# Kernel tuning notes

Measured on AMD Instinct MI355X. Metric: run time of the kernel, lower is better.

## Reference

```python
import jax, jax.numpy as jnp
import numpy as np

N_HEADS = 16
LEVELS = 3
DS = 2          # downsampling_factor
WINDOW = 128    # sliding window size
B, L, E = 32, 512, 1024


def _mha(q, k, v, Wq, bq, Wk, bk, Wv, bv, Wo, bo):
    """batch_first nn.MultiheadAttention equivalent (no mask)."""
    b, lq, e = q.shape
    lk = k.shape[1]
    d = e // N_HEADS
    scale = 1.0 / np.sqrt(d)
    qh = (q @ Wq + bq).reshape(b, lq, N_HEADS, d)
    kh = (k @ Wk + bk).reshape(b, lk, N_HEADS, d)
    vh = (v @ Wv + bv).reshape(b, lk, N_HEADS, d)
    att = jax.nn.softmax(jnp.einsum('bqhd,bkhd->bhqk', qh, kh) * scale, axis=-1)
    out = jnp.einsum('bhqk,bkhd->bqhd', att, vh).reshape(b, lq, e)
    return out @ Wo + bo


def _downsample(x):
    b, l, e = x.shape
    ln = l // DS
    return x[:, :ln * DS].reshape(b, ln, DS, e).mean(axis=2)


def setup_inputs() -> dict:
    key = jax.random.key(0)
    ks = jax.random.split(key, 8)
    s = E ** -0.5
    return {
        'query': jax.random.normal(ks[0], (B, L, E), jnp.float32),
        'key': jax.random.normal(ks[1], (B, L, E), jnp.float32),
        'value': jax.random.normal(ks[2], (B, L, E), jnp.float32),
        'Wq': jax.random.normal(ks[3], (E, E), jnp.float32) * s,
        'bq': jnp.zeros((E,), jnp.float32),
        'Wk': jax.random.normal(ks[4], (E, E), jnp.float32) * s,
        'bk': jnp.zeros((E,), jnp.float32),
        'Wv': jax.random.normal(ks[5], (E, E), jnp.float32) * s,
        'bv': jnp.zeros((E,), jnp.float32),
        'Wo': jax.random.normal(ks[6], (E, E), jnp.float32) * s,
        'bo': jnp.zeros((E,), jnp.float32),
        'soft_mask': jnp.ones((L,), jnp.float32),
    }


def reference(query, key, value, Wq, bq, Wk, bk, Wv, bv, Wo, bo, soft_mask):
    params = (Wq, bq, Wk, bk, Wv, bv, Wo, bo)
    # hierarchical multi-scale attention: full KV + (levels-1) downsampled KVs
    k, v = key, value
    acc = _mha(query, k, v, *params)
    for _ in range(LEVELS - 1):
        k = _downsample(k)
        v = _downsample(v)
        acc = acc + _mha(query, k, v, *params)
    hier = acc / LEVELS
    # sliding-window local attention (L divisible by WINDOW)
    b, l, e = query.shape
    nw = l // WINDOW
    qw = query.reshape(b * nw, WINDOW, e)
    kw = key.reshape(b * nw, WINDOW, e)
    vw = value.reshape(b * nw, WINDOW, e)
    sw = _mha(qw, kw, vw, *params).reshape(b, l, e)
    # soft mask gating
    sm = jax.nn.sigmoid(soft_mask[:l])
    return (hier + sw) * sm[None, :, None]
```

## Files before the change

### kernel.cpp

```cpp
#include <hip/hip_runtime.h>

#define EDIM 1024
#define MROWS 16384
#define DHEAD 64
#define LSEQ 512
#define NT 16
#define QSCL 0.125f

typedef unsigned short u16;
typedef unsigned int u32;
typedef __bf16 bf16x8 __attribute__((ext_vector_type(8)));
typedef unsigned short u16x8 __attribute__((ext_vector_type(8)));
typedef float f32x4 __attribute__((ext_vector_type(4)));

__device__ __forceinline__ u16 f2bf(float x) {
    return __builtin_bit_cast(u16, (__bf16)x);
}
__device__ __forceinline__ float bf2f(u16 h) {
    return __builtin_bit_cast(float, (u32)h << 16);
}
__device__ __forceinline__ bf16x8 ld8(const u16* p) {
    return __builtin_bit_cast(bf16x8, *(const u16x8*)p);
}
__device__ __forceinline__ bf16x8 ld8s(const u16* base, int row, int koff) {
    return ld8((const u16*)((const char*)base + row * 128 + ((koff * 2) ^ ((row & 7) << 4))));
}
__device__ __forceinline__ bf16x8 ld8v(const u16* base, int c, int koff) {
    return ld8((const u16*)((const char*)base + c * 128 + ((koff * 2) ^ (((c >> 2) & 7) << 4))));
}
__device__ __forceinline__ void glds16(const u16* g, u16* l) {
    __builtin_amdgcn_global_load_lds(
        (const __attribute__((address_space(1))) u32*)g,
        (__attribute__((address_space(3))) u32*)l, 16, 0, 0);
}
__device__ __forceinline__ u32 pk2(float a, float b) {
    return (u32)f2bf(a) | ((u32)f2bf(b) << 16);
}
__device__ __forceinline__ u32 dup2(float a) {
    u32 v = (u32)f2bf(a); return v | (v << 16);
}
#define MFMA(a, b, c) __builtin_amdgcn_mfma_f32_16x16x32_bf16((a), (b), (c), 0, 0, 0)
#define U4C(v, i) ((i) == 0 ? (v).x : (i) == 1 ? (v).y : (i) == 2 ? (v).z : (v).w)
#define VMCNT(n) asm volatile("s_waitcnt vmcnt(" #n ")" ::: "memory")
#define SBAR()   __builtin_amdgcn_s_barrier()

__global__ __launch_bounds__(256) void prep_wt_kernel(
    const float* __restrict__ Wq, const float* __restrict__ Wk,
    const float* __restrict__ Wv, const float* __restrict__ Wo,
    u16* __restrict__ WTh)
{
    const int z = blockIdx.z;
    const float* W = (z == 0) ? Wq : (z == 1) ? Wk : (z == 2) ? Wv : Wo;
    const float scl = (z == 0) ? QSCL : 1.0f;
    u16* th = WTh + (size_t)z * EDIM * EDIM;
    const int k0 = blockIdx.x * 64, n0 = blockIdx.y * 64;
    __shared__ float tile[64][65];
    for (int i = threadIdx.x; i < 4096; i += 256) {
        int r = i >> 6, c = i & 63;
        tile[r][c] = W[(size_t)(k0 + r) * EDIM + n0 + c];
    }
    __syncthreads();
    for (int i = threadIdx.x; i < 4096; i += 256) {
        int r = i >> 6, c = i & 63;
        th[(size_t)(n0 + r) * EDIM + k0 + c] = f2bf(tile[c][r] * scl);
    }
}

__global__ __launch_bounds__(256) void convert_kernel(
    const float* __restrict__ Aq, const float* __restrict__ Ak, const float* __restrict__ Av,
    u16* __restrict__ Dq, u16* __restrict__ Dk, u16* __restrict__ Dv)
{
    const int z = blockIdx.z;
    const float* src = (z == 0) ? Aq : (z == 1) ? Ak : Av;
    u16* dst = (z == 0) ? Dq : (z == 1) ? Dk : Dv;
    const size_t total8 = (size_t)MROWS * EDIM / 8;
    for (size_t i = (size_t)blockIdx.x * 256 + threadIdx.x; i < total8;
         i += (size_t)gridDim.x * 256) {
        const float4 a = *(const float4*)&src[i * 8];
        const float4 b = *(const float4*)&src[i * 8 + 4];
        ushort4 h0, h1;
        h0.x = f2bf(a.x); h0.y = f2bf(a.y); h0.z = f2bf(a.z); h0.w = f2bf(a.w);
        h1.x = f2bf(b.x); h1.y = f2bf(b.y); h1.z = f2bf(b.z); h1.w = f2bf(b.w);
        *(ushort4*)&dst[i * 8]     = h0;
        *(ushort4*)&dst[i * 8 + 4] = h1;
    }
}

template<int EPI>
__global__ __launch_bounds__(512, 1) void gemm256(
    const u16* __restrict__ A, const u16* __restrict__ BT,
    const float* __restrict__ bias, float bsc,
    u16* __restrict__ Ch, float* __restrict__ Cf, const float* __restrict__ smask)
{
    extern __shared__ u16 lds[];
    const int tid = threadIdx.x;
    const int lane = tid & 63, w = tid >> 6;
    const int wm = w >> 2, wn = w & 3;
    const int lr = lane & 15, lg = lane >> 4;
    int D = blockIdx.x;
    int T = (D & 7) * 32 + (D >> 3);
    const int m0 = (T >> 2) * 256, n0 = (T & 3) * 256;

    u16* As0 = lds;
    u16* As1 = lds + 16384;
    u16* Bs0 = lds + 32768;
    u16* Bs1 = lds + 49152;

    auto stageB = [&](int bf, int t) {
        u16* dst = bf ? Bs1 : Bs0;
        #pragma unroll
        for (int c = 0; c < 4; ++c) {
            int idx = tid + c * 512;
            int row = idx >> 3, ch = idx & 7, sch = ch ^ (row & 7);
            glds16(&BT[(size_t)(n0 + row) * EDIM + t * 64 + sch * 8], dst + idx * 8);
        }
    };
    auto stageA = [&](int bf, int t) {
        u16* dst = bf ? As1 : As0;
        #pragma unroll
        for (int c = 0; c < 4; ++c) {
            int idx = tid + c * 512;
            int row = idx >> 3, ch = idx & 7, sch = ch ^ (row & 7);
            glds16(&A[(size_t)(m0 + row) * EDIM + t * 64 + sch * 8], dst + idx * 8);
        }
    };

    f32x4 acc[8][4] = {};
    bf16x8 bf0[4], bf1[4];

    stageB(0, 0);
    stageA(0, 0);
    VMCNT(0);
    SBAR();
    #pragma unroll
    for (int n = 0; n < 4; ++n)
        bf0[n] = ld8s(Bs0, wn * 64 + n * 16 + lr, lg * 8);

    for (int t = 0; t < NT; ++t) {
        const int cur = t & 1;
        u16* Asc = cur ? As1 : As0;
        u16* Bsc = cur ? Bs1 : Bs0;
        u16* Bsn = cur ? Bs0 : Bs1;
        const bool more = (t + 1 < NT);
        bf16x8 af[4];
        #pragma unroll
        for (int mm = 0; mm < 4; ++mm)
            af[mm] = ld8s(Asc, wm * 128 + mm * 16 + lr, lg * 8);
        if (more) { stageB(cur ^ 1, t + 1); stageA(cur ^ 1, t + 1); }
        SBAR();
        __builtin_amdgcn_s_setprio(1);
        #pragma unroll
        for (int n = 0; n < 4; ++n)
            #pragma unroll
            for (int mm = 0; mm < 4; ++mm)
                acc[mm][n] = MFMA(af[mm], bf0[n], acc[mm][n]);
        __builtin_amdgcn_s_setprio(0);
        SBAR();
        bf16x8 ag[4];
        #pragma unroll
        for (int mm = 0; mm < 4; ++mm)
            ag[mm] = ld8s(Asc, wm * 128 + 64 + mm * 16 + lr, lg * 8);
        SBAR();
        __builtin_amdgcn_s_setprio(1);
        #pragma unroll
        for (int n = 0; n < 4; ++n)
            #pragma unroll
            for (int mm = 0; mm < 4; ++mm)
                acc[4 + mm][n] = MFMA(ag[mm], bf0[n], acc[4 + mm][n]);
        __builtin_amdgcn_s_setprio(0);
        SBAR();
        #pragma unroll
        for (int mm = 0; mm < 4; ++mm)
            af[mm] = ld8s(Asc, wm * 128 + mm * 16 + lr, 32 + lg * 8);
        #pragma unroll
        for (int n = 0; n < 4; ++n)
            bf1[n] = ld8s(Bsc, wn * 64 + n * 16 + lr, 32 + lg * 8);
        SBAR();
        __builtin_amdgcn_s_setprio(1);
        #pragma unroll
        for (int n = 0; n < 4; ++n)
            #pragma unroll
            for (int mm = 0; mm < 4; ++mm)
                acc[mm][n] = MFMA(af[mm], bf1[n], acc[mm][n]);
        __builtin_amdgcn_s_setprio(0);
        VMCNT(4);
        SBAR();
        #pragma unroll
        for (int mm = 0; mm < 4; ++mm)
            ag[mm] = ld8s(Asc, wm * 128 + 64 + mm * 16 + lr, 32 + lg * 8);
        if (more) {
            #pragma unroll
            for (int n = 0; n < 4; ++n)
                bf0[n] = ld8s(Bsn, wn * 64 + n * 16 + lr, lg * 8);
        }
        SBAR();
        __builtin_amdgcn_s_setprio(1);
        #pragma unroll
        for (int n = 0; n < 4; ++n)
            #pragma unroll
            for (int mm = 0; mm < 4; ++mm)
                acc[4 + mm][n] = MFMA(ag[mm], bf1[n], acc[4 + mm][n]);
        __builtin_amdgcn_s_setprio(0);
        VMCNT(0);
        SBAR();
    }
    #pragma unroll
    for (int m = 0; m < 8; ++m)
        #pragma unroll
        for (int n = 0; n < 4; ++n) {
            int col = n0 + wn * 64 + n * 16 + lr;
            float bc = bias[col];
            #pragma unroll
            for (int r = 0; r < 4; ++r) {
                int row = m0 + wm * 128 + m * 16 + lg * 4 + r;
                float x = acc[m][n][r];
                if (EPI == 1) {
                    float g = 1.0f / (1.0f + __expf(-smask[row & (LSEQ - 1)]));
                    Cf[(size_t)row * EDIM + col] = (x + 2.0f * bc) * g;
                } else {
                    Ch[(size_t)row * EDIM + col] = f2bf(x + bsc * bc);
                }
            }
        }
}

__global__ __launch_bounds__(512, 2) void attn_kernel(
    const u16* __restrict__ Q, const u16* __restrict__ K,
    const u16* __restrict__ V, u16* __restrict__ ctx)
{
    __shared__ u16 Ks[2][64 * 64];
    __shared__ u16 Vt[64 * 64];
    __shared__ u16 Ps[8][16 * 72];
    const int tid = threadIdx.x, lane = tid & 63, w = tid >> 6;
    const int lr = lane & 15, lg = lane >> 4;
    int D = blockIdx.x;
    int T = (D & 7) * 256 + (D >> 3);
    const int qq = T & 3, hd = (T >> 2) & 15, b = T >> 6;
    const int wrow = b * LSEQ + qq * 128 + w * 16;
    const int ecol = hd * DHEAD;
    const int kvbase = b * LSEQ;
    const int wt0 = qq * 2;

    char* psw = (char*)&Ps[w][0];

    bf16x8 qf0 = ld8(&Q[(size_t)(wrow + lr) * EDIM + ecol + lg * 8]);
    bf16x8 qf1 = ld8(&Q[(size_t)(wrow + lr) * EDIM + ecol + 32 + lg * 8]);

    f32x4 o0[4] = {}, o1[4] = {}, o2[4] = {}, ow[4] = {};
    float l0 = 0, l1 = 0, l2 = 0, lw = 0;
    ushort4 vr0, vr1;

    auto issueK = [&](int t, int bf) {
        int row = tid >> 3, ch = tid & 7, sch = ch ^ (row & 7);
        glds16(&K[(size_t)(kvbase + t * 64 + row) * EDIM + ecol + sch * 8],
               &Ks[bf][w * 512]);
    };
    auto loadV = [&](int t) {
        int pr = tid >> 4, c4 = (tid & 15) << 2;
        vr0 = *(const ushort4*)&V[(size_t)(kvbase + t * 64 + 2 * pr) * EDIM + ecol + c4];
        vr1 = *(const ushort4*)&V[(size_t)(kvbase + t * 64 + 2 * pr + 1) * EDIM + ecol + c4];
    };
    auto writeV = [&]() {
        int pr = tid >> 4, c4 = (tid & 15) << 2;
        #pragma unroll
        for (int i = 0; i < 4; ++i) {
            int c = c4 + i;
            int byo = c * 128 + ((4 * pr) ^ (((c >> 2) & 7) << 4));
            *(u32*)((char*)Vt + byo) = (u32)U4C(vr0, i) | ((u32)U4C(vr1, i) << 16);
        }
    };

    int buf = 0;
    issueK(0, 0);
    loadV(0);
    for (int t = 0; t < 8; ++t) {
        __syncthreads();
        writeV();
        __syncthreads();
        if (t < 7) { issueK(t + 1, buf ^ 1); loadV(t + 1); }
        const bool win = (t == wt0) | (t == wt0 + 1);
        u16* Ksc = &Ks[buf][0];

        f32x4 s[4];
        #pragma unroll
        for (int nb = 0; nb < 4; ++nb) {
            bf16x8 kf0 = ld8s(Ksc, nb * 16 + lr, lg * 8);
            bf16x8 kf1 = ld8s(Ksc, nb * 16 + lr, 32 + lg * 8);
            f32x4 a = {};
            a = MFMA(kf0, qf0, a);
            a = MFMA(kf1, qf1, a);
            s[nb] = a;
        }
        float l0t = 0;
        #pragma unroll
        for (int nb = 0; nb < 4; ++nb) {
            float p0 = __expf(s[nb][0]), p1 = __expf(s[nb][1]);
            float p2 = __expf(s[nb][2]), p3 = __expf(s[nb][3]);
            l0t += (p0 + p1) + (p2 + p3);
            char* pb = psw + lr * 144 + nb * 32 + lg * 8;
            *(u32*)pb       = pk2(p0, p1);
            *(u32*)(pb + 4) = pk2(p2, p3);
        }
        l0 += l0t;
        if (win) lw += l0t;
        {
            bf16x8 pa0 = ld8((const u16*)(psw + lr * 144 + lg * 16));
            bf16x8 pa1 = ld8((const u16*)(psw + lr * 144 + 64 + lg * 16));
            #pragma unroll
            for (int nd = 0; nd < 4; ++nd) {
                bf16x8 vb0 = ld8v(Vt, nd * 16 + lr, lg * 8);
                bf16x8 vb1 = ld8v(Vt, nd * 16 + lr, 32 + lg * 8);
                o0[nd] = MFMA(pa0, vb0, o0[nd]);
                o0[nd] = MFMA(pa1, vb1, o0[nd]);
                if (win) {
                    ow[nd] = MFMA(pa0, vb0, ow[nd]);
                    ow[nd] = MFMA(pa1, vb1, ow[nd]);
                }
            }
        }
        float s1[4][2];
        #pragma unroll
        for (int nb = 0; nb < 4; ++nb) {
            s1[nb][0] = 0.5f * (s[nb][0] + s[nb][1]);
            s1[nb][1] = 0.5f * (s[nb][2] + s[nb][3]);
            float pa = __expf(s1[nb][0]), pc = __expf(s1[nb][1]);
            l1 += pa + pc;
            char* pb = psw + lr * 144 + nb * 32 + lg * 8;
            *(u32*)pb       = dup2(pa);
            *(u32*)(pb + 4) = dup2(pc);
        }
        {
            bf16x8 pa0 = ld8((const u16*)(psw + lr * 144 + lg * 16));
            bf16x8 pa1 = ld8((const u16*)(psw + lr * 144 + 64 + lg * 16));
            #pragma unroll
            for (int nd = 0; nd < 4; ++nd) {
                bf16x8 vb0 = ld8v(Vt, nd * 16 + lr, lg * 8);
                bf16x8 vb1 = ld8v(Vt, nd * 16 + lr, 32 + lg * 8);
                o1[nd] = MFMA(pa0, vb0, o1[nd]);
                o1[nd] = MFMA(pa1, vb1, o1[nd]);
            }
        }
        #pragma unroll
        for (int nb = 0; nb < 4; ++nb) {
            float pv = __expf(0.5f * (s1[nb][0] + s1[nb][1]));
            l2 += pv;
            char* pb = psw + lr * 144 + nb * 32 + lg * 8;
            u32 d = dup2(pv);
            *(u32*)pb       = d;
            *(u32*)(pb + 4) = d;
        }
        {
            bf16x8 pa0 = ld8((const u16*)(psw + lr * 144 + lg * 16));
            bf16x8 pa1 = ld8((const u16*)(psw + lr * 144 + 64 + lg * 16));
            #pragma unroll
            for (int nd = 0; nd < 4; ++nd) {
                bf16x8 vb0 = ld8v(Vt, nd * 16 + lr, lg * 8);
                bf16x8 vb1 = ld8v(Vt, nd * 16 + lr, 32 + lg * 8);
                o2[nd] = MFMA(pa0, vb0, o2[nd]);
                o2[nd] = MFMA(pa1, vb1, o2[nd]);
            }
        }
        buf ^= 1;
    }
    l0 += __shfl_xor(l0, 16, 64); l0 += __shfl_xor(l0, 32, 64);
    l1 += __shfl_xor(l1, 16, 64); l1 += __shfl_xor(l1, 32, 64);
    l2 += __shfl_xor(l2, 16, 64); l2 += __shfl_xor(l2, 32, 64);
    lw += __shfl_xor(lw, 16, 64); lw += __shfl_xor(lw, 32, 64);
    float c0 = (1.0f / 3.0f) / l0;
    float c1 = (1.0f / 6.0f) / l1;
    float c2 = (1.0f / 12.0f) / l2;
    float cw = 1.0f / lw;
    #pragma unroll
    for (int r = 0; r < 4; ++r) {
        int src = lg * 4 + r;
        float d0 = __shfl(c0, src, 64);
        float d1 = __shfl(c1, src, 64);
        float d2 = __shfl(c2, src, 64);
        float dw = __shfl(cw, src, 64);
        #pragma unroll
        for (int nd = 0; nd < 4; ++nd) {
            float v = o0[nd][r] * d0 + o1[nd][r] * d1 + o2[nd][r] * d2 + ow[nd][r] * dw;
            ctx[(size_t)(wrow + lg * 4 + r) * EDIM + ecol + nd * 16 + lr] = f2bf(v);
        }
    }
}

extern "C" void kernel_launch(void* const* d_in, const int* in_sizes, int n_in,
                              void* d_out, int out_size, void* d_ws, size_t ws_size,
                              hipStream_t stream)
{
    const float* query = (const float*)d_in[0];
    const float* key   = (const float*)d_in[1];
    const float* value = (const float*)d_in[2];
    const float* Wq = (const float*)d_in[3];
    const float* bq = (const float*)d_in[4];
    const float* Wk = (const float*)d_in[5];
    const float* bk = (const float*)d_in[6];
    const float* Wv = (const float*)d_in[7];
    const float* bv = (const float*)d_in[8];
    const float* Wo = (const float*)d_in[9];
    const float* bo = (const float*)d_in[10];
    const float* smask = (const float*)d_in[11];

    const size_t szWT = (size_t)4 * EDIM * EDIM * 2;
    const size_t szP  = (size_t)MROWS * EDIM * 2;
    const size_t need = szWT + 7 * szP;
    if (ws_size < need) {
        hipMemsetAsync(d_out, 0x7F, (size_t)out_size * 4, stream);
        return;
    }
    size_t off = 0;
    auto take = [&](size_t n) -> void* {
        void* p = (char*)d_ws + off;
        off += (n + 255) & ~(size_t)255;
        return p;
    };
    u16* WTh = (u16*)take(szWT);
    u16* Aq  = (u16*)take(szP);
    u16* Ak  = (u16*)take(szP);
    u16* Av  = (u16*)take(szP);
    u16* Qh  = (u16*)take(szP);
    u16* Kh  = (u16*)take(szP);
    u16* Vh  = (u16*)take(szP);
    u16* ctx = (u16*)take(szP);

    (void)hipFuncSetAttribute(reinterpret_cast<const void*>(gemm256<0>),
                              hipFuncAttributeMaxDynamicSharedMemorySize, 131072);
    (void)hipFuncSetAttribute(reinterpret_cast<const void*>(gemm256<1>),
                              hipFuncAttributeMaxDynamicSharedMemorySize, 131072);

    prep_wt_kernel<<<dim3(16, 16, 4), 256, 0, stream>>>(Wq, Wk, Wv, Wo, WTh);
    convert_kernel<<<dim3(4096, 1, 3), 256, 0, stream>>>(query, key, value, Aq, Ak, Av);

    gemm256<0><<<256, 512, 131072, stream>>>(
        Aq, WTh + 0 * (size_t)EDIM * EDIM, bq, QSCL, Qh, nullptr, nullptr);
    gemm256<0><<<256, 512, 131072, stream>>>(
        Ak, WTh + 1 * (size_t)EDIM * EDIM, bk, 1.0f, Kh, nullptr, nullptr);
    gemm256<0><<<256, 512, 131072, stream>>>(
        Av, WTh + 2 * (size_t)EDIM * EDIM, bv, 1.0f, Vh, nullptr, nullptr);

    attn_kernel<<<2048, 512, 0, stream>>>(Qh, Kh, Vh, ctx);

    gemm256<1><<<256, 512, 131072, stream>>>(
        ctx, WTh + 3 * (size_t)EDIM * EDIM, bo, 1.0f, nullptr, (float*)d_out, smask);
}
```

Measured before the change: 389.4 us.

## Fuse fp32-to-bf16 input conversion into projection GEMMs and fold log2e into Q scale

Removes the separate convert kernel: the Q/K/V projection GEMMs now load fp32 activations into registers, convert them to bf16, and write them swizzled into LDS, so the bf16 copies are never stored to memory and read back. The Q scale now includes log2(e), so the attention kernel uses exp2f. It derives the probabilities for the downsampled levels from sqrt of products of the fine-level ones instead of recomputing exponentials. In exchange the GEMM A path no longer uses async global-to-LDS loads, waits on vmcnt(0) every step and holds more registers, which may weaken its pipelining.

```diff
diff --git a/kernel.cpp b/kernel.cpp
--- a/kernel.cpp
+++ b/kernel.cpp
@@ -5,7 +5,7 @@
 #define DHEAD 64
 #define LSEQ 512
 #define NT 16
-#define QSCL 0.125f
+#define QSCL 0.18033688011112042f
 
 typedef unsigned short u16;
 typedef unsigned int u32;
@@ -42,6 +42,7 @@
 #define MFMA(a, b, c) __builtin_amdgcn_mfma_f32_16x16x32_bf16((a), (b), (c), 0, 0, 0)
 #define U4C(v, i) ((i) == 0 ? (v).x : (i) == 1 ? (v).y : (i) == 2 ? (v).z : (v).w)
 #define VMCNT(n) asm volatile("s_waitcnt vmcnt(" #n ")" ::: "memory")
+#define LGKM0()  asm volatile("s_waitcnt lgkmcnt(0)" ::: "memory")
 #define SBAR()   __builtin_amdgcn_s_barrier()
 
 __global__ __launch_bounds__(256) void prep_wt_kernel(
@@ -66,29 +67,10 @@
     }
 }
 
-__global__ __launch_bounds__(256) void convert_kernel(
-    const float* __restrict__ Aq, const float* __restrict__ Ak, const float* __restrict__ Av,
-    u16* __restrict__ Dq, u16* __restrict__ Dk, u16* __restrict__ Dv)
-{
-    const int z = blockIdx.z;
-    const float* src = (z == 0) ? Aq : (z == 1) ? Ak : Av;
-    u16* dst = (z == 0) ? Dq : (z == 1) ? Dk : Dv;
-    const size_t total8 = (size_t)MROWS * EDIM / 8;
-    for (size_t i = (size_t)blockIdx.x * 256 + threadIdx.x; i < total8;
-         i += (size_t)gridDim.x * 256) {
-        const float4 a = *(const float4*)&src[i * 8];
-        const float4 b = *(const float4*)&src[i * 8 + 4];
-        ushort4 h0, h1;
-        h0.x = f2bf(a.x); h0.y = f2bf(a.y); h0.z = f2bf(a.z); h0.w = f2bf(a.w);
-        h1.x = f2bf(b.x); h1.y = f2bf(b.y); h1.z = f2bf(b.z); h1.w = f2bf(b.w);
-        *(ushort4*)&dst[i * 8]     = h0;
-        *(ushort4*)&dst[i * 8 + 4] = h1;
-    }
-}
-
-template<int EPI>
+template<int EPI, int AF32>
 __global__ __launch_bounds__(512, 1) void gemm256(
-    const u16* __restrict__ A, const u16* __restrict__ BT,
+    const float* __restrict__ Af, const u16* __restrict__ Ah,
+    const u16* __restrict__ BT,
     const float* __restrict__ bias, float bsc,
     u16* __restrict__ Ch, float* __restrict__ Cf, const float* __restrict__ smask)
 {
@@ -121,7 +103,26 @@
         for (int c = 0; c < 4; ++c) {
             int idx = tid + c * 512;
             int row = idx >> 3, ch = idx & 7, sch = ch ^ (row & 7);
-            glds16(&A[(size_t)(m0 + row) * EDIM + t * 64 + sch * 8], dst + idx * 8);
+            glds16(&Ah[(size_t)(m0 + row) * EDIM + t * 64 + sch * 8], dst + idx * 8);
+        }
+    };
+    float4 ar[8];
+    auto loadA = [&](int t) {
+        #pragma unroll
+        for (int j = 0; j < 8; ++j) {
+            int row = j * 32 + (tid >> 4), c4 = (tid & 15) << 2;
+            ar[j] = *(const float4*)&Af[(size_t)(m0 + row) * EDIM + t * 64 + c4];
+        }
+    };
+    auto writeA = [&](int bf) {
+        u16* dst = bf ? As1 : As0;
+        #pragma unroll
+        for (int j = 0; j < 8; ++j) {
+            int row = j * 32 + (tid >> 4), c4 = (tid & 15) << 2;
+            ushort4 h;
+            h.x = f2bf(ar[j].x); h.y = f2bf(ar[j].y);
+            h.z = f2bf(ar[j].z); h.w = f2bf(ar[j].w);
+            *(ushort4*)((char*)dst + row * 128 + ((c4 * 2) ^ ((row & 7) << 4))) = h;
         }
     };
 
@@ -129,8 +130,9 @@
     bf16x8 bf0[4], bf1[4];
 
     stageB(0, 0);
-    stageA(0, 0);
+    if constexpr (AF32) loadA(0); else stageA(0, 0);
     VMCNT(0);
+    if constexpr (AF32) { writeA(0); LGKM0(); }
     SBAR();
     #pragma unroll
     for (int n = 0; n < 4; ++n)
@@ -146,7 +148,10 @@
         #pragma unroll
         for (int mm = 0; mm < 4; ++mm)
             af[mm] = ld8s(Asc, wm * 128 + mm * 16 + lr, lg * 8);
-        if (more) { stageB(cur ^ 1, t + 1); stageA(cur ^ 1, t + 1); }
+        if (more) {
+            stageB(cur ^ 1, t + 1);
+            if constexpr (AF32) loadA(t + 1); else stageA(cur ^ 1, t + 1);
+        }
         SBAR();
         __builtin_amdgcn_s_setprio(1);
         #pragma unroll
@@ -183,7 +188,7 @@
             for (int mm = 0; mm < 4; ++mm)
                 acc[mm][n] = MFMA(af[mm], bf1[n], acc[mm][n]);
         __builtin_amdgcn_s_setprio(0);
-        VMCNT(4);
+        if constexpr (AF32) VMCNT(0); else VMCNT(4);
         SBAR();
         #pragma unroll
         for (int mm = 0; mm < 4; ++mm)
@@ -202,6 +207,9 @@
                 acc[4 + mm][n] = MFMA(ag[mm], bf1[n], acc[4 + mm][n]);
         __builtin_amdgcn_s_setprio(0);
         VMCNT(0);
+        if constexpr (AF32) {
+            if (more) { writeA(cur ^ 1); LGKM0(); }
+        }
         SBAR();
     }
     #pragma unroll
@@ -291,15 +299,19 @@
             a = MFMA(kf1, qf1, a);
             s[nb] = a;
         }
+        float pa[4], pc[4], pv[4];
         float l0t = 0;
         #pragma unroll
         for (int nb = 0; nb < 4; ++nb) {
-            float p0 = __expf(s[nb][0]), p1 = __expf(s[nb][1]);
-            float p2 = __expf(s[nb][2]), p3 = __expf(s[nb][3]);
+            float p0 = exp2f(s[nb][0]), p1 = exp2f(s[nb][1]);
+            float p2 = exp2f(s[nb][2]), p3 = exp2f(s[nb][3]);
             l0t += (p0 + p1) + (p2 + p3);
-            char* pb = psw + lr * 144 + nb * 32 + lg * 8;
-            *(u32*)pb       = pk2(p0, p1);
-            *(u32*)(pb + 4) = pk2(p2, p3);
+            pa[nb] = sqrtf(p0 * p1); pc[nb] = sqrtf(p2 * p3);
+            l1 += pa[nb] + pc[nb];
+            pv[nb] = sqrtf(pa[nb] * pc[nb]);
+            l2 += pv[nb];
+            uint2 u; u.x = pk2(p0, p1); u.y = pk2(p2, p3);
+            *(uint2*)(psw + lr * 144 + nb * 32 + lg * 8) = u;
         }
         l0 += l0t;
         if (win) lw += l0t;
@@ -318,16 +330,10 @@
                 }
             }
         }
-        float s1[4][2];
         #pragma unroll
         for (int nb = 0; nb < 4; ++nb) {
-            s1[nb][0] = 0.5f * (s[nb][0] + s[nb][1]);
-            s1[nb][1] = 0.5f * (s[nb][2] + s[nb][3]);
-            float pa = __expf(s1[nb][0]), pc = __expf(s1[nb][1]);
-            l1 += pa + pc;
-            char* pb = psw + lr * 144 + nb * 32 + lg * 8;
-            *(u32*)pb       = dup2(pa);
-            *(u32*)(pb + 4) = dup2(pc);
+            uint2 u; u.x = dup2(pa[nb]); u.y = dup2(pc[nb]);
+            *(uint2*)(psw + lr * 144 + nb * 32 + lg * 8) = u;
         }
         {
             bf16x8 pa0 = ld8((const u16*)(psw + lr * 144 + lg * 16));
@@ -342,12 +348,9 @@
         }
         #pragma unroll
         for (int nb = 0; nb < 4; ++nb) {
-            float pv = __expf(0.5f * (s1[nb][0] + s1[nb][1]));
-            l2 += pv;
-            char* pb = psw + lr * 144 + nb * 32 + lg * 8;
-            u32 d = dup2(pv);
-            *(u32*)pb       = d;
-            *(u32*)(pb + 4) = d;
+            u32 d = dup2(pv[nb]);
+            uint2 u; u.x = d; u.y = d;
+            *(uint2*)(psw + lr * 144 + nb * 32 + lg * 8) = u;
         }
         {
             bf16x8 pa0 = ld8((const u16*)(psw + lr * 144 + lg * 16));
@@ -404,7 +407,7 @@
 
     const size_t szWT = (size_t)4 * EDIM * EDIM * 2;
     const size_t szP  = (size_t)MROWS * EDIM * 2;
-    const size_t need = szWT + 7 * szP;
+    const size_t need = szWT + 4 * szP;
     if (ws_size < need) {
         hipMemsetAsync(d_out, 0x7F, (size_t)out_size * 4, stream);
         return;
@@ -416,31 +419,27 @@
         return p;
     };
     u16* WTh = (u16*)take(szWT);
-    u16* Aq  = (u16*)take(szP);
-    u16* Ak  = (u16*)take(szP);
-    u16* Av  = (u16*)take(szP);
     u16* Qh  = (u16*)take(szP);
     u16* Kh  = (u16*)take(szP);
     u16* Vh  = (u16*)take(szP);
     u16* ctx = (u16*)take(szP);
 
-    (void)hipFuncSetAttribute(reinterpret_cast<const void*>(gemm256<0>),
+    (void)hipFuncSetAttribute(reinterpret_cast<const void*>(gemm256<0, 1>),
                               hipFuncAttributeMaxDynamicSharedMemorySize, 131072);
-    (void)hipFuncSetAttribute(reinterpret_cast<const void*>(gemm256<1>),
+    (void)hipFuncSetAttribute(reinterpret_cast<const void*>(gemm256<1, 0>),
                               hipFuncAttributeMaxDynamicSharedMemorySize, 131072);
 
     prep_wt_kernel<<<dim3(16, 16, 4), 256, 0, stream>>>(Wq, Wk, Wv, Wo, WTh);
-    convert_kernel<<<dim3(4096, 1, 3), 256, 0, stream>>>(query, key, value, Aq, Ak, Av);
-
-    gemm256<0><<<256, 512, 131072, stream>>>(
-        Aq, WTh + 0 * (size_t)EDIM * EDIM, bq, QSCL, Qh, nullptr, nullptr);
-    gemm256<0><<<256, 512, 131072, stream>>>(
-        Ak, WTh + 1 * (size_t)EDIM * EDIM, bk, 1.0f, Kh, nullptr, nullptr);
-    gemm256<0><<<256, 512, 131072, stream>>>(
-        Av, WTh + 2 * (size_t)EDIM * EDIM, bv, 1.0f, Vh, nullptr, nullptr);
+
+    gemm256<0, 1><<<256, 512, 131072, stream>>>(
+        query, nullptr, WTh + 0 * (size_t)EDIM * EDIM, bq, QSCL, Qh, nullptr, nullptr);
+    gemm256<0, 1><<<256, 512, 131072, stream>>>(
+        key,   nullptr, WTh + 1 * (size_t)EDIM * EDIM, bk, 1.0f, Kh, nullptr, nullptr);
+    gemm256<0, 1><<<256, 512, 131072, stream>>>(
+        value, nullptr, WTh + 2 * (size_t)EDIM * EDIM, bv, 1.0f, Vh, nullptr, nullptr);
 
     attn_kernel<<<2048, 512, 0, stream>>>(Qh, Kh, Vh, ctx);
 
-    gemm256<1><<<256, 512, 131072, stream>>>(
-        ctx, WTh + 3 * (size_t)EDIM * EDIM, bo, 1.0f, nullptr, (float*)d_out, smask);
-}
+    gemm256<1, 0><<<256, 512, 131072, stream>>>(
+        nullptr, ctx, WTh + 3 * (size_t)EDIM * EDIM, bo, 1.0f, nullptr, (float*)d_out, smask);
+}
```

Result: no change. 386.1 us (-0.9%).
